# Performance work log

Hardware: AMD Instinct MI355X
Metric: run time of the kernel (lower is better)

Reference implementation:

```python
import jax, jax.numpy as jnp
import numpy as np

B, N, D, DN, F, NUM_F, O, H = 8, 4096, 256, 128, 128, 1024, 8, 1024
EPS = 1e-5

def setup_inputs() -> dict:
    key = jax.random.key(0)
    ks = jax.random.split(key, 10)
    s = 0.02
    x = jax.random.normal(ks[0], (B, N, D), dtype=jnp.float32)
    ctx = jax.random.normal(ks[1], (B, DN), dtype=jnp.float32)
    idx = jax.random.randint(ks[2], (F,), 0, NUM_F, dtype=jnp.int64)
    cond_w = jax.random.normal(ks[3], (DN, 2 * D), dtype=jnp.float32) * s
    cond_b = jnp.zeros((2 * D,), dtype=jnp.float32)
    ffn_w_in = jax.random.normal(ks[4], (D, 2 * H), dtype=jnp.float32) * s
    ffn_b_in = jnp.zeros((2 * H,), dtype=jnp.float32)
    ffn_w_out = jax.random.normal(ks[5], (H, D), dtype=jnp.float32) * s
    ffn_b_out = jnp.zeros((D,), dtype=jnp.float32)
    emb = jax.random.normal(ks[6], (NUM_F, D * O), dtype=jnp.float32) * s
    return {"x": x, "ctx": ctx, "idx": idx, "cond_w": cond_w, "cond_b": cond_b,
            "ffn_w_in": ffn_w_in, "ffn_b_in": ffn_b_in,
            "ffn_w_out": ffn_w_out, "ffn_b_out": ffn_b_out, "emb": emb}

def reference(x, ctx, idx, cond_w, cond_b, ffn_w_in, ffn_b_in, ffn_w_out, ffn_b_out, emb):
    # Conditional LayerNorm: normalize over last dim, FiLM-style modulation from ctx
    mu = jnp.mean(x, axis=-1, keepdims=True)
    var = jnp.mean((x - mu) ** 2, axis=-1, keepdims=True)
    h = (x - mu) * jax.lax.rsqrt(var + EPS)                      # [B,N,D]
    ss = ctx @ cond_w + cond_b                                   # [B,2D]
    scale, shift = jnp.split(ss, 2, axis=-1)                     # [B,D] each
    h = h * (1.0 + scale[:, None, :]) + shift[:, None, :]
    # Gated FFN: in-proj -> (gelu(gate) * value) -> out-proj
    uv = h @ ffn_w_in + ffn_b_in                                 # [B,N,2H]
    u, v = jnp.split(uv, 2, axis=-1)
    y = (jax.nn.gelu(u) * v) @ ffn_w_out + ffn_b_out             # [B,N,D]
    # Embedding-generated per-feature output weights, then batched contraction
    w = emb[idx].reshape(F, D, O)                                # gather [F,D,O]
    out = jnp.einsum('bnd,fdo->bnfo', y, w)                      # [B,N,F,O]
    return out
```

## Files before the change

### kernel.cpp

```cpp
#include <hip/hip_runtime.h>
#include <cstdint>
#include <cstddef>

#define M_TOT 32768
#define D_    256
#define DN_   128
#define TWO_D 512
#define H_    1024
#define TWO_H 2048

typedef unsigned short ushort_t;
typedef __attribute__((ext_vector_type(8))) short bf16x8;
typedef __attribute__((ext_vector_type(4))) float f32x4;

__device__ __forceinline__ ushort_t f2bf(float f) {
  union { float f; uint32_t i; } v; v.f = f;
  uint32_t r = v.i + 0x7fffu + ((v.i >> 16) & 1u);
  return (ushort_t)(r >> 16);
}

__device__ __forceinline__ void async_ld16(const void* g, void* l) {
  __builtin_amdgcn_global_load_lds(
      (const __attribute__((address_space(1))) void*)g,
      (__attribute__((address_space(3))) void*)l, 16, 0, 0);
}

__global__ __launch_bounds__(256) void cond_ss_kernel(
    const float* __restrict__ ctx, const float* __restrict__ cond_w,
    const float* __restrict__ cond_b, float* __restrict__ ss) {
  int j = blockIdx.x * 256 + threadIdx.x;
  int b = j >> 9, col = j & 511;
  float acc = cond_b[col];
  for (int k = 0; k < DN_; ++k)
    acc += ctx[b * DN_ + k] * cond_w[k * TWO_D + col];
  ss[j] = acc;
}

__global__ __launch_bounds__(256) void transpose_f32_bf16_kernel(
    const float* __restrict__ in, ushort_t* __restrict__ out, int R, int C) {
  __shared__ float T[64 * 65];
  int ctiles = C >> 6;
  int bi = blockIdx.x / ctiles, bj = blockIdx.x % ctiles;
  int r0 = bi * 64, c0 = bj * 64;
  int tid = threadIdx.x;
#pragma unroll
  for (int it = 0; it < 16; ++it) {
    int idx = it * 256 + tid;
    int r = idx >> 6, c = idx & 63;
    T[r * 65 + c] = in[(size_t)(r0 + r) * C + c0 + c];
  }
  __syncthreads();
#pragma unroll
  for (int it = 0; it < 8; ++it) {
    int idx = it * 256 + tid;
    int a = idx >> 5;
    int b = (idx & 31) * 2;
    uint32_t pk = (uint32_t)f2bf(T[b * 65 + a]) |
                  ((uint32_t)f2bf(T[(b + 1) * 65 + a]) << 16);
    *(uint32_t*)&out[(size_t)(c0 + a) * R + r0 + b] = pk;
  }
}

__global__ __launch_bounds__(256) void gather_emb_kernel(
    const float* __restrict__ emb, const int* __restrict__ idx,
    ushort_t* __restrict__ W2T) {
  int f = blockIdx.x;
  bool looks64 = (idx[1] == 0) & (idx[3] == 0) & (idx[5] == 0) & (idx[7] == 0);
  int fi = looks64 ? idx[2 * f] : idx[f];
  const float* src = emb + (size_t)fi * 2048;
  int o = threadIdx.x >> 5, d0 = (threadIdx.x & 31) * 8;
  ushort_t buf[8];
#pragma unroll
  for (int k = 0; k < 8; ++k) buf[k] = f2bf(src[(d0 + k) * 8 + o]);
  *(bf16x8*)&W2T[(size_t)(f * 8 + o) * 256 + d0] = *(bf16x8*)buf;
}

__global__ __launch_bounds__(256) void ln_film_kernel(
    const float* __restrict__ x, const float* __restrict__ ss,
    ushort_t* __restrict__ h) {
  int row = blockIdx.x * 4 + (threadIdx.x >> 6);
  int lane = threadIdx.x & 63;
  int b = row >> 12;
  const float* xr = x + (size_t)row * D_;
  float4 pk = *(const float4*)(xr + lane * 4);
  float f0 = pk.x, f1 = pk.y, f2 = pk.z, f3 = pk.w;
  float s = f0 + f1 + f2 + f3;
  float q = f0 * f0 + f1 * f1 + f2 * f2 + f3 * f3;
#pragma unroll
  for (int off = 32; off > 0; off >>= 1) {
    s += __shfl_xor(s, off, 64);
    q += __shfl_xor(q, off, 64);
  }
  float mean = s * (1.0f / 256.0f);
  float var = q * (1.0f / 256.0f) - mean * mean;
  float rs = rsqrtf(var + 1e-5f);
  int d = lane * 4;
  const float* ssb = ss + b * TWO_D;
  float o0 = (f0 - mean) * rs * (1.0f + ssb[d + 0]) + ssb[256 + d + 0];
  float o1 = (f1 - mean) * rs * (1.0f + ssb[d + 1]) + ssb[256 + d + 1];
  float o2 = (f2 - mean) * rs * (1.0f + ssb[d + 2]) + ssb[256 + d + 2];
  float o3 = (f3 - mean) * rs * (1.0f + ssb[d + 3]) + ssb[256 + d + 3];
  uint2 st;
  st.x = (uint32_t)f2bf(o0) | ((uint32_t)f2bf(o1) << 16);
  st.y = (uint32_t)f2bf(o2) | ((uint32_t)f2bf(o3) << 16);
  *(uint2*)(h + (size_t)row * D_ + lane * 4) = st;
}

__global__ __launch_bounds__(512, 2) void ffn_fused_kernel(
    const ushort_t* __restrict__ h,
    const ushort_t* __restrict__ WinT,
    const float* __restrict__ bin,
    const ushort_t* __restrict__ WoutT,
    const float* __restrict__ bout,
    ushort_t* __restrict__ y) {
  __shared__ ushort_t S3[3][8192];
  __shared__ ushort_t Gs[128 * 72];
  __shared__ float Lbin[2048];
  const int tid = threadIdx.x, lane = tid & 63, wave = tid >> 6;
  const int wm = wave >> 1, wn = wave & 1;
  const int r = lane >> 2, q = lane & 3;
  const int qs = q ^ ((r >> 1) & 3);
  const int l15 = lane & 15, l4 = lane >> 4;
  const int m0 = blockIdx.x * 128;
  const int fragoff = l15 * 32 + (l4 ^ ((l15 >> 1) & 3)) * 8;

  const char* winb  = (const char*)WinT  + r * 512 + qs * 16;
  const char* woutb = (const char*)WoutT + r * 2048 + qs * 16;

  const ushort_t* hp = h + (size_t)(m0 + wm * 32 + l15) * 256 + l4 * 8;
  bf16x8 a_reg[2][8];
#pragma unroll
  for (int rt = 0; rt < 2; ++rt)
#pragma unroll
    for (int kc = 0; kc < 8; ++kc)
      a_reg[rt][kc] = *(const bf16x8*)(hp + rt * 4096 + kc * 32);

  async_ld16((const char*)bin + wave * 1024 + lane * 16,
             (char*)Lbin + wave * 1024);

  auto stage_in = [&](ushort_t* dst, int jrow, int k0e) {
#pragma unroll
    for (int i = 0; i < 2; ++i) {
      int tt = i * 8 + wave;
      int vv = tt >> 3, t7 = tt & 7;
      int ks = t7 >> 2, cc = t7 & 3;
      async_ld16(winb + (size_t)vv * 524288 + jrow * 32768 + cc * 8192 +
                     k0e * 2 + ks * 64,
                 &dst[tt * 512]);
    }
  };
  auto stage_wout = [&](ushort_t* dst, int jrow, int s2) {
#pragma unroll
    for (int i = 0; i < 2; ++i) {
      int tt = i * 8 + wave;
      async_ld16(woutb + (size_t)tt * 32768 + jrow * 128 + s2 * 64,
                 &dst[tt * 512]);
    }
  };

  stage_in(S3[0], 0, 0);
  stage_in(S3[1], 0, 64);

  f32x4 yac[2][8] = {};

#define ENTRY2()                                        \
  asm volatile("s_waitcnt vmcnt(2)" ::: "memory");      \
  __builtin_amdgcn_s_barrier();                         \
  asm volatile("" ::: "memory");
#define ENTRY2L()                                                  \
  asm volatile("s_waitcnt vmcnt(2) lgkmcnt(0)" ::: "memory");      \
  __builtin_amdgcn_s_barrier();                                    \
  asm volatile("" ::: "memory");

#define MFMA_IN(buf, p_)                                                      \
  {                                                                           \
    const ushort_t* cur_ = (buf);                                             \
    __builtin_amdgcn_s_setprio(1);                                            \
    _Pragma("unroll")                                                         \
    for (int ks = 0; ks < 2; ++ks) {                                          \
      _Pragma("unroll")                                                       \
      for (int jj = 0; jj < 2; ++jj) {                                        \
        int tt = ks * 4 + wn * 2 + jj;                                        \
        bf16x8 bu = *(const bf16x8*)&cur_[tt * 512 + fragoff];                \
        bf16x8 bv = *(const bf16x8*)&cur_[(8 + tt) * 512 + fragoff];          \
        uac[0][jj] = __builtin_amdgcn_mfma_f32_16x16x32_bf16(a_reg[0][(p_)*2+ks], bu, uac[0][jj], 0, 0, 0); \
        uac[1][jj] = __builtin_amdgcn_mfma_f32_16x16x32_bf16(a_reg[1][(p_)*2+ks], bu, uac[1][jj], 0, 0, 0); \
        vac[0][jj] = __builtin_amdgcn_mfma_f32_16x16x32_bf16(a_reg[0][(p_)*2+ks], bv, vac[0][jj], 0, 0, 0); \
        vac[1][jj] = __builtin_amdgcn_mfma_f32_16x16x32_bf16(a_reg[1][(p_)*2+ks], bv, vac[1][jj], 0, 0, 0); \
      }                                                                       \
    }                                                                         \
    __builtin_amdgcn_s_setprio(0);                                            \
  }

#define MFMA_OUT(buf, s2_)                                                    \
  {                                                                           \
    const ushort_t* cur_ = (buf);                                             \
    bf16x8 gf0 = *(const bf16x8*)&Gs[(wm * 32 + l15) * 72 + (s2_) * 32 + l4 * 8];      \
    bf16x8 gf1 = *(const bf16x8*)&Gs[(wm * 32 + 16 + l15) * 72 + (s2_) * 32 + l4 * 8]; \
    __builtin_amdgcn_s_setprio(1);                                            \
    _Pragma("unroll")                                                         \
    for (int nt8 = 0; nt8 < 8; ++nt8) {                                       \
      bf16x8 bw = *(const bf16x8*)&cur_[(wn * 8 + nt8) * 512 + fragoff];      \
      yac[0][nt8] = __builtin_amdgcn_mfma_f32_16x16x32_bf16(gf0, bw, yac[0][nt8], 0, 0, 0); \
      yac[1][nt8] = __builtin_amdgcn_mfma_f32_16x16x32_bf16(gf1, bw, yac[1][nt8], 0, 0, 0); \
    }                                                                         \
    __builtin_amdgcn_s_setprio(0);                                            \
  }

  for (int j = 0; j < 16; ++j) {
    const int jn = (j + 1) & 15;
    f32x4 uac[2][2] = {}, vac[2][2] = {};

    ENTRY2(); stage_in(S3[2], j, 128);  MFMA_IN(S3[0], 0);
    ENTRY2(); stage_in(S3[0], j, 192);  MFMA_IN(S3[1], 1);
    ENTRY2(); stage_wout(S3[1], j, 0);  MFMA_IN(S3[2], 2);
    ENTRY2(); stage_wout(S3[2], j, 1);  MFMA_IN(S3[0], 3);

#pragma unroll
    for (int jj = 0; jj < 2; ++jj) {
      int gcol = wn * 32 + jj * 16 + l15;
      float bub = Lbin[j * 64 + gcol];
      float bvb = Lbin[1024 + j * 64 + gcol];
#pragma unroll
      for (int rt = 0; rt < 2; ++rt) {
#pragma unroll
        for (int rr = 0; rr < 4; ++rr) {
          float u = uac[rt][jj][rr] + bub;
          float v = vac[rt][jj][rr] + bvb;
          float t = 0.7978845608028654f * (u + 0.044715f * u * u * u);
          float e = __expf(2.0f * t);
          float th = 1.0f - 2.0f / (e + 1.0f);
          float gl = 0.5f * u * (1.0f + th);
          Gs[(wm * 32 + rt * 16 + l4 * 4 + rr) * 72 + gcol] = f2bf(gl * v);
        }
      }
    }

    ENTRY2L(); stage_in(S3[0], jn, 0);  MFMA_OUT(S3[1], 0);
    ENTRY2();  stage_in(S3[1], jn, 64); MFMA_OUT(S3[2], 1);
  }

  asm volatile("s_waitcnt vmcnt(0)" ::: "memory");
  __builtin_amdgcn_s_barrier();
  asm volatile("" ::: "memory");
  ushort_t* E = &S3[0][0];
#pragma unroll
  for (int hh = 0; hh < 2; ++hh) {
    if ((wm >> 1) == hh) {
      int er0 = (wm & 1) * 32;
#pragma unroll
      for (int nt8 = 0; nt8 < 8; ++nt8) {
        int col = wn * 128 + nt8 * 16 + l15;
        float bb = bout[col];
#pragma unroll
        for (int rt = 0; rt < 2; ++rt)
#pragma unroll
          for (int rr = 0; rr < 4; ++rr)
            E[(er0 + rt * 16 + l4 * 4 + rr) * 264 + col] = f2bf(yac[rt][nt8][rr] + bb);
      }
    }
    asm volatile("s_waitcnt lgkmcnt(0)" ::: "memory");
    __builtin_amdgcn_s_barrier();
    asm volatile("" ::: "memory");
#pragma unroll
    for (int it = 0; it < 4; ++it) {
      int id = it * 512 + tid;
      int rr = id >> 5, cc = id & 31;
      bf16x8 vv = *(const bf16x8*)&E[rr * 264 + cc * 8];
      *(bf16x8*)&y[(size_t)(m0 + hh * 64 + rr) * 256 + cc * 8] = vv;
    }
    if (hh == 0) {
      __builtin_amdgcn_s_barrier();
      asm volatile("" ::: "memory");
    }
  }
#undef ENTRY2
#undef ENTRY2L
#undef MFMA_IN
#undef MFMA_OUT
}

__global__ __launch_bounds__(256, 2) void gemm_out_kernel(
    const ushort_t* __restrict__ A, const ushort_t* __restrict__ BT,
    float* __restrict__ C) {
  __shared__ ushort_t SB[2][16384];
  const int tid = threadIdx.x, lane = tid & 63, wave = tid >> 6;
  const int wm = wave >> 1, wn = wave & 1;
  const int m0 = blockIdx.x * 128, n0 = blockIdx.y * 128;
  const int r = lane >> 2, q = lane & 3;
  const int qs = q ^ ((r >> 1) & 3);
  const int l15 = lane & 15, l4 = lane >> 4;
  const int fragoff = l15 * 32 + (l4 ^ ((l15 >> 1) & 3)) * 8;
  const int N = 1024, K = 256;

  auto stage = [&](ushort_t* dst, int k0) {
#pragma unroll
    for (int i = 0; i < 4; ++i) {
      int t = i * 4 + wave;
      int rt = t >> 1, ks = t & 1;
      async_ld16(A + (size_t)(m0 + rt * 16 + r) * K + k0 + ks * 32 + qs * 8, &dst[t * 512]);
      async_ld16(BT + (size_t)(n0 + rt * 16 + r) * K + k0 + ks * 32 + qs * 8, &dst[(16 + t) * 512]);
    }
  };

  f32x4 acc[4][4] = {};
  stage(SB[0], 0);
#pragma unroll
  for (int ki = 0; ki < 4; ++ki) {
    __builtin_amdgcn_s_barrier();
    asm volatile("" ::: "memory");
    if (ki < 3) {
      stage(SB[(ki + 1) & 1], (ki + 1) * 64);
      asm volatile("s_waitcnt vmcnt(8)" ::: "memory");
    } else {
      asm volatile("s_waitcnt vmcnt(0)" ::: "memory");
    }
    __builtin_amdgcn_s_barrier();
    asm volatile("" ::: "memory");
    const ushort_t* cur = SB[ki & 1];
    __builtin_amdgcn_s_setprio(1);
#pragma unroll
    for (int ks = 0; ks < 2; ++ks) {
      bf16x8 a[4], b[4];
#pragma unroll
      for (int i = 0; i < 4; ++i)
        a[i] = *(const bf16x8*)&cur[((wm * 4 + i) * 2 + ks) * 512 + fragoff];
#pragma unroll
      for (int jt = 0; jt < 4; ++jt)
        b[jt] = *(const bf16x8*)&cur[(16 + (wn * 4 + jt) * 2 + ks) * 512 + fragoff];
#pragma unroll
      for (int i = 0; i < 4; ++i)
#pragma unroll
        for (int jt = 0; jt < 4; ++jt)
          acc[i][jt] = __builtin_amdgcn_mfma_f32_16x16x32_bf16(a[i], b[jt], acc[i][jt], 0, 0, 0);
    }
    __builtin_amdgcn_s_setprio(0);
  }
#pragma unroll
  for (int jt = 0; jt < 4; ++jt) {
    int col = n0 + wn * 64 + jt * 16 + l15;
#pragma unroll
    for (int i = 0; i < 4; ++i) {
      int row = m0 + wm * 64 + i * 16 + l4 * 4;
#pragma unroll
      for (int rr = 0; rr < 4; ++rr)
        C[(size_t)(row + rr) * N + col] = acc[i][jt][rr];
    }
  }
}

extern "C" void kernel_launch(void* const* d_in, const int* in_sizes, int n_in,
                              void* d_out, int out_size, void* d_ws, size_t ws_size,
                              hipStream_t stream) {
  const float* x      = (const float*)d_in[0];
  const float* ctx    = (const float*)d_in[1];
  const int*   idx    = (const int*)d_in[2];
  const float* cond_w = (const float*)d_in[3];
  const float* cond_b = (const float*)d_in[4];
  const float* w_in   = (const float*)d_in[5];
  const float* b_in   = (const float*)d_in[6];
  const float* w_out  = (const float*)d_in[7];
  const float* b_out  = (const float*)d_in[8];
  const float* emb    = (const float*)d_in[9];

  char* w = (char*)d_ws;
  float* ss = (float*)w;           w += (size_t)8 * TWO_D * 4;
  ushort_t* h = (ushort_t*)w;      w += (size_t)M_TOT * D_ * 2;
  ushort_t* y = (ushort_t*)w;      w += (size_t)M_TOT * D_ * 2;
  ushort_t* WinT = (ushort_t*)w;   w += (size_t)TWO_H * D_ * 2;
  ushort_t* WoutT = (ushort_t*)w;  w += (size_t)D_ * H_ * 2;
  ushort_t* W2T = (ushort_t*)w;    w += (size_t)H_ * D_ * 2;

  cond_ss_kernel<<<16, 256, 0, stream>>>(ctx, cond_w, cond_b, ss);
  transpose_f32_bf16_kernel<<<(D_ / 64) * (TWO_H / 64), 256, 0, stream>>>(w_in, WinT, D_, TWO_H);
  transpose_f32_bf16_kernel<<<(H_ / 64) * (D_ / 64), 256, 0, stream>>>(w_out, WoutT, H_, D_);
  gather_emb_kernel<<<128, 256, 0, stream>>>(emb, idx, W2T);
  ln_film_kernel<<<M_TOT / 4, 256, 0, stream>>>(x, ss, h);
  ffn_fused_kernel<<<M_TOT / 128, 512, 0, stream>>>(h, WinT, b_in, WoutT, b_out, y);
  gemm_out_kernel<<<dim3(M_TOT / 128, H_ / 128), 256, 0, stream>>>(y, W2T, (float*)d_out);
}
```

Before: 292.9 us.

## Retile FFN waves to 2x4 grid and stage final GEMM output via LDS

Changes the FFN kernel's wave layout from 4x2 to 2x4, so each wave holds 64 rows of A in registers and covers fewer columns. This gives each B fragment load from LDS more MFMA reuse in both the in-projection and out-projection. It also rewrites the final contraction GEMM epilogue to stage fp32 accumulators through shared memory and write coalesced float4 rows, in place of scattered scalar stores. The cost is more A registers per wave (which may hurt occupancy at launch bounds 512,2) and extra barriers in the epilogue.

```diff
diff --git a/kernel.cpp b/kernel.cpp
--- a/kernel.cpp
+++ b/kernel.cpp
@@ -117,7 +117,7 @@
   __shared__ ushort_t Gs[128 * 72];
   __shared__ float Lbin[2048];
   const int tid = threadIdx.x, lane = tid & 63, wave = tid >> 6;
-  const int wm = wave >> 1, wn = wave & 1;
+  const int wm = wave >> 2, wn = wave & 3;
   const int r = lane >> 2, q = lane & 3;
   const int qs = q ^ ((r >> 1) & 3);
   const int l15 = lane & 15, l4 = lane >> 4;
@@ -127,10 +127,10 @@
   const char* winb  = (const char*)WinT  + r * 512 + qs * 16;
   const char* woutb = (const char*)WoutT + r * 2048 + qs * 16;
 
-  const ushort_t* hp = h + (size_t)(m0 + wm * 32 + l15) * 256 + l4 * 8;
-  bf16x8 a_reg[2][8];
-#pragma unroll
-  for (int rt = 0; rt < 2; ++rt)
+  const ushort_t* hp = h + (size_t)(m0 + wm * 64 + l15) * 256 + l4 * 8;
+  bf16x8 a_reg[4][8];
+#pragma unroll
+  for (int rt = 0; rt < 4; ++rt)
 #pragma unroll
     for (int kc = 0; kc < 8; ++kc)
       a_reg[rt][kc] = *(const bf16x8*)(hp + rt * 4096 + kc * 32);
@@ -161,7 +161,7 @@
   stage_in(S3[0], 0, 0);
   stage_in(S3[1], 0, 64);
 
-  f32x4 yac[2][8] = {};
+  f32x4 yac[4][4] = {};
 
 #define ENTRY2()                                        \
   asm volatile("s_waitcnt vmcnt(2)" ::: "memory");      \
@@ -178,15 +178,13 @@
     __builtin_amdgcn_s_setprio(1);                                            \
     _Pragma("unroll")                                                         \
     for (int ks = 0; ks < 2; ++ks) {                                          \
+      int tt = ks * 4 + wn;                                                   \
+      bf16x8 bu = *(const bf16x8*)&cur_[tt * 512 + fragoff];                  \
+      bf16x8 bv = *(const bf16x8*)&cur_[(8 + tt) * 512 + fragoff];            \
       _Pragma("unroll")                                                       \
-      for (int jj = 0; jj < 2; ++jj) {                                        \
-        int tt = ks * 4 + wn * 2 + jj;                                        \
-        bf16x8 bu = *(const bf16x8*)&cur_[tt * 512 + fragoff];                \
-        bf16x8 bv = *(const bf16x8*)&cur_[(8 + tt) * 512 + fragoff];          \
-        uac[0][jj] = __builtin_amdgcn_mfma_f32_16x16x32_bf16(a_reg[0][(p_)*2+ks], bu, uac[0][jj], 0, 0, 0); \
-        uac[1][jj] = __builtin_amdgcn_mfma_f32_16x16x32_bf16(a_reg[1][(p_)*2+ks], bu, uac[1][jj], 0, 0, 0); \
-        vac[0][jj] = __builtin_amdgcn_mfma_f32_16x16x32_bf16(a_reg[0][(p_)*2+ks], bv, vac[0][jj], 0, 0, 0); \
-        vac[1][jj] = __builtin_amdgcn_mfma_f32_16x16x32_bf16(a_reg[1][(p_)*2+ks], bv, vac[1][jj], 0, 0, 0); \
+      for (int rt = 0; rt < 4; ++rt) {                                        \
+        uac[rt] = __builtin_amdgcn_mfma_f32_16x16x32_bf16(a_reg[rt][(p_)*2+ks], bu, uac[rt], 0, 0, 0); \
+        vac[rt] = __builtin_amdgcn_mfma_f32_16x16x32_bf16(a_reg[rt][(p_)*2+ks], bv, vac[rt], 0, 0, 0); \
       }                                                                       \
     }                                                                         \
     __builtin_amdgcn_s_setprio(0);                                            \
@@ -195,43 +193,45 @@
 #define MFMA_OUT(buf, s2_)                                                    \
   {                                                                           \
     const ushort_t* cur_ = (buf);                                             \
-    bf16x8 gf0 = *(const bf16x8*)&Gs[(wm * 32 + l15) * 72 + (s2_) * 32 + l4 * 8];      \
-    bf16x8 gf1 = *(const bf16x8*)&Gs[(wm * 32 + 16 + l15) * 72 + (s2_) * 32 + l4 * 8]; \
+    bf16x8 gf[4];                                                             \
+    _Pragma("unroll")                                                         \
+    for (int rt = 0; rt < 4; ++rt)                                            \
+      gf[rt] = *(const bf16x8*)&Gs[(wm * 64 + rt * 16 + l15) * 72 + (s2_) * 32 + l4 * 8]; \
     __builtin_amdgcn_s_setprio(1);                                            \
     _Pragma("unroll")                                                         \
-    for (int nt8 = 0; nt8 < 8; ++nt8) {                                       \
-      bf16x8 bw = *(const bf16x8*)&cur_[(wn * 8 + nt8) * 512 + fragoff];      \
-      yac[0][nt8] = __builtin_amdgcn_mfma_f32_16x16x32_bf16(gf0, bw, yac[0][nt8], 0, 0, 0); \
-      yac[1][nt8] = __builtin_amdgcn_mfma_f32_16x16x32_bf16(gf1, bw, yac[1][nt8], 0, 0, 0); \
+    for (int nt = 0; nt < 4; ++nt) {                                          \
+      bf16x8 bw = *(const bf16x8*)&cur_[(wn * 4 + nt) * 512 + fragoff];       \
+      _Pragma("unroll")                                                       \
+      for (int rt = 0; rt < 4; ++rt)                                          \
+        yac[rt][nt] = __builtin_amdgcn_mfma_f32_16x16x32_bf16(gf[rt], bw, yac[rt][nt], 0, 0, 0); \
     }                                                                         \
     __builtin_amdgcn_s_setprio(0);                                            \
   }
 
   for (int j = 0; j < 16; ++j) {
     const int jn = (j + 1) & 15;
-    f32x4 uac[2][2] = {}, vac[2][2] = {};
+    f32x4 uac[4] = {}, vac[4] = {};
 
     ENTRY2(); stage_in(S3[2], j, 128);  MFMA_IN(S3[0], 0);
     ENTRY2(); stage_in(S3[0], j, 192);  MFMA_IN(S3[1], 1);
     ENTRY2(); stage_wout(S3[1], j, 0);  MFMA_IN(S3[2], 2);
     ENTRY2(); stage_wout(S3[2], j, 1);  MFMA_IN(S3[0], 3);
 
-#pragma unroll
-    for (int jj = 0; jj < 2; ++jj) {
-      int gcol = wn * 32 + jj * 16 + l15;
+    {
+      int gcol = wn * 16 + l15;
       float bub = Lbin[j * 64 + gcol];
       float bvb = Lbin[1024 + j * 64 + gcol];
 #pragma unroll
-      for (int rt = 0; rt < 2; ++rt) {
+      for (int rt = 0; rt < 4; ++rt) {
 #pragma unroll
         for (int rr = 0; rr < 4; ++rr) {
-          float u = uac[rt][jj][rr] + bub;
-          float v = vac[rt][jj][rr] + bvb;
+          float u = uac[rt][rr] + bub;
+          float v = vac[rt][rr] + bvb;
           float t = 0.7978845608028654f * (u + 0.044715f * u * u * u);
           float e = __expf(2.0f * t);
           float th = 1.0f - 2.0f / (e + 1.0f);
           float gl = 0.5f * u * (1.0f + th);
-          Gs[(wm * 32 + rt * 16 + l4 * 4 + rr) * 72 + gcol] = f2bf(gl * v);
+          Gs[(wm * 64 + rt * 16 + l4 * 4 + rr) * 72 + gcol] = f2bf(gl * v);
         }
       }
     }
@@ -246,17 +246,16 @@
   ushort_t* E = &S3[0][0];
 #pragma unroll
   for (int hh = 0; hh < 2; ++hh) {
-    if ((wm >> 1) == hh) {
-      int er0 = (wm & 1) * 32;
-#pragma unroll
-      for (int nt8 = 0; nt8 < 8; ++nt8) {
-        int col = wn * 128 + nt8 * 16 + l15;
+    if (wm == hh) {
+#pragma unroll
+      for (int nt = 0; nt < 4; ++nt) {
+        int col = wn * 64 + nt * 16 + l15;
         float bb = bout[col];
 #pragma unroll
-        for (int rt = 0; rt < 2; ++rt)
+        for (int rt = 0; rt < 4; ++rt)
 #pragma unroll
           for (int rr = 0; rr < 4; ++rr)
-            E[(er0 + rt * 16 + l4 * 4 + rr) * 264 + col] = f2bf(yac[rt][nt8][rr] + bb);
+            E[(rt * 16 + l4 * 4 + rr) * 264 + col] = f2bf(yac[rt][nt][rr] + bb);
       }
     }
     asm volatile("s_waitcnt lgkmcnt(0)" ::: "memory");
@@ -336,15 +335,33 @@
     }
     __builtin_amdgcn_s_setprio(0);
   }
-#pragma unroll
-  for (int jt = 0; jt < 4; ++jt) {
-    int col = n0 + wn * 64 + jt * 16 + l15;
-#pragma unroll
-    for (int i = 0; i < 4; ++i) {
-      int row = m0 + wm * 64 + i * 16 + l4 * 4;
-#pragma unroll
-      for (int rr = 0; rr < 4; ++rr)
-        C[(size_t)(row + rr) * N + col] = acc[i][jt][rr];
+  float* Cs = (float*)&SB[0][0];
+#pragma unroll
+  for (int p = 0; p < 2; ++p) {
+    __builtin_amdgcn_s_barrier();
+    asm volatile("" ::: "memory");
+    if (wm == p) {
+#pragma unroll
+      for (int jt = 0; jt < 4; ++jt) {
+        int col = wn * 64 + jt * 16 + l15;
+#pragma unroll
+        for (int i = 0; i < 4; ++i) {
+          int rl = i * 16 + (l4 << 2);
+#pragma unroll
+          for (int rr = 0; rr < 4; ++rr)
+            Cs[(rl + rr) * 132 + col] = acc[i][jt][rr];
+        }
+      }
+    }
+    asm volatile("s_waitcnt lgkmcnt(0)" ::: "memory");
+    __builtin_amdgcn_s_barrier();
+    asm volatile("" ::: "memory");
+#pragma unroll
+    for (int it = 0; it < 8; ++it) {
+      int t = it * 256 + tid;
+      int rr = t >> 5, c = (t & 31) * 4;
+      float4 v = *(const float4*)&Cs[rr * 132 + c];
+      *(float4*)&C[(size_t)(m0 + p * 64 + rr) * N + n0 + c] = v;
     }
   }
 }
```

After: 305.3 us. +4.2%, slower.

## Merge prep kernels and restructure output GEMM with coalesced LDS-staged stores

Applied to the files above, without the earlier changes.

The four small preprocessing kernels (cond projection, two weight transposes, embedding gather) become one launch, with blocks dispatched by index, to cut launch overhead. The output GEMM drops LDS double-buffered async staging and loads fragments straight from global memory. Each block now covers 64x256 instead of 128x128, and accumulators go through an LDS tile so the fp32 output is written as coalesced float4 rows rather than scattered scalar stores. The output write is the dominant traffic at 128 MB. The cost is more global read traffic for A/B fragments without LDS reuse, plus extra LDS round trips and barriers in the epilogue.

```diff
diff --git a/kernel.cpp b/kernel.cpp
--- a/kernel.cpp
+++ b/kernel.cpp
@@ -25,24 +25,12 @@
       (__attribute__((address_space(3))) void*)l, 16, 0, 0);
 }
 
-__global__ __launch_bounds__(256) void cond_ss_kernel(
-    const float* __restrict__ ctx, const float* __restrict__ cond_w,
-    const float* __restrict__ cond_b, float* __restrict__ ss) {
-  int j = blockIdx.x * 256 + threadIdx.x;
-  int b = j >> 9, col = j & 511;
-  float acc = cond_b[col];
-  for (int k = 0; k < DN_; ++k)
-    acc += ctx[b * DN_ + k] * cond_w[k * TWO_D + col];
-  ss[j] = acc;
-}
-
-__global__ __launch_bounds__(256) void transpose_f32_bf16_kernel(
-    const float* __restrict__ in, ushort_t* __restrict__ out, int R, int C) {
-  __shared__ float T[64 * 65];
+__device__ __forceinline__ void transpose_body(
+    const float* __restrict__ in, ushort_t* __restrict__ out, int R, int C,
+    int bb, int tid, float* T) {
   int ctiles = C >> 6;
-  int bi = blockIdx.x / ctiles, bj = blockIdx.x % ctiles;
+  int bi = bb / ctiles, bj = bb % ctiles;
   int r0 = bi * 64, c0 = bj * 64;
-  int tid = threadIdx.x;
 #pragma unroll
   for (int it = 0; it < 16; ++it) {
     int idx = it * 256 + tid;
@@ -61,18 +49,37 @@
   }
 }
 
-__global__ __launch_bounds__(256) void gather_emb_kernel(
+__global__ __launch_bounds__(256) void prep_kernel(
+    const float* __restrict__ ctx, const float* __restrict__ cond_w,
+    const float* __restrict__ cond_b, float* __restrict__ ss,
+    const float* __restrict__ w_in, ushort_t* __restrict__ WinT,
+    const float* __restrict__ w_out, ushort_t* __restrict__ WoutT,
     const float* __restrict__ emb, const int* __restrict__ idx,
     ushort_t* __restrict__ W2T) {
-  int f = blockIdx.x;
-  bool looks64 = (idx[1] == 0) & (idx[3] == 0) & (idx[5] == 0) & (idx[7] == 0);
-  int fi = looks64 ? idx[2 * f] : idx[f];
-  const float* src = emb + (size_t)fi * 2048;
-  int o = threadIdx.x >> 5, d0 = (threadIdx.x & 31) * 8;
-  ushort_t buf[8];
-#pragma unroll
-  for (int k = 0; k < 8; ++k) buf[k] = f2bf(src[(d0 + k) * 8 + o]);
-  *(bf16x8*)&W2T[(size_t)(f * 8 + o) * 256 + d0] = *(bf16x8*)buf;
+  __shared__ float T[64 * 65];
+  int bid = blockIdx.x, tid = threadIdx.x;
+  if (bid < 16) {
+    int j = bid * 256 + tid;
+    int b = j >> 9, col = j & 511;
+    float acc = cond_b[col];
+    for (int k = 0; k < DN_; ++k)
+      acc += ctx[b * DN_ + k] * cond_w[k * TWO_D + col];
+    ss[j] = acc;
+  } else if (bid < 144) {
+    transpose_body(w_in, WinT, D_, TWO_H, bid - 16, tid, T);
+  } else if (bid < 208) {
+    transpose_body(w_out, WoutT, H_, D_, bid - 144, tid, T);
+  } else {
+    int f = bid - 208;
+    bool looks64 = (idx[1] == 0) & (idx[3] == 0) & (idx[5] == 0) & (idx[7] == 0);
+    int fi = looks64 ? idx[2 * f] : idx[f];
+    const float* src = emb + (size_t)fi * 2048;
+    int o = tid >> 5, d0 = (tid & 31) * 8;
+    ushort_t buf[8];
+#pragma unroll
+    for (int k = 0; k < 8; ++k) buf[k] = f2bf(src[(d0 + k) * 8 + o]);
+    *(bf16x8*)&W2T[(size_t)(f * 8 + o) * 256 + d0] = *(bf16x8*)buf;
+  }
 }
 
 __global__ __launch_bounds__(256) void ln_film_kernel(
@@ -280,71 +287,54 @@
 #undef MFMA_OUT
 }
 
-__global__ __launch_bounds__(256, 2) void gemm_out_kernel(
+__global__ __launch_bounds__(256, 4) void gemm_out_kernel(
     const ushort_t* __restrict__ A, const ushort_t* __restrict__ BT,
     float* __restrict__ C) {
-  __shared__ ushort_t SB[2][16384];
+  __shared__ float Cs[32 * 260];
   const int tid = threadIdx.x, lane = tid & 63, wave = tid >> 6;
-  const int wm = wave >> 1, wn = wave & 1;
-  const int m0 = blockIdx.x * 128, n0 = blockIdx.y * 128;
-  const int r = lane >> 2, q = lane & 3;
-  const int qs = q ^ ((r >> 1) & 3);
   const int l15 = lane & 15, l4 = lane >> 4;
-  const int fragoff = l15 * 32 + (l4 ^ ((l15 >> 1) & 3)) * 8;
-  const int N = 1024, K = 256;
-
-  auto stage = [&](ushort_t* dst, int k0) {
-#pragma unroll
-    for (int i = 0; i < 4; ++i) {
-      int t = i * 4 + wave;
-      int rt = t >> 1, ks = t & 1;
-      async_ld16(A + (size_t)(m0 + rt * 16 + r) * K + k0 + ks * 32 + qs * 8, &dst[t * 512]);
-      async_ld16(BT + (size_t)(n0 + rt * 16 + r) * K + k0 + ks * 32 + qs * 8, &dst[(16 + t) * 512]);
-    }
-  };
-
+  const int m0 = blockIdx.y * 64;
+  const int n0 = blockIdx.x * 256;
+  const ushort_t* Ap = A + (size_t)(m0 + l15) * 256 + l4 * 8;
+  const ushort_t* Bp = BT + (size_t)(n0 + wave * 64 + l15) * 256 + l4 * 8;
   f32x4 acc[4][4] = {};
-  stage(SB[0], 0);
-#pragma unroll
-  for (int ki = 0; ki < 4; ++ki) {
-    __builtin_amdgcn_s_barrier();
-    asm volatile("" ::: "memory");
-    if (ki < 3) {
-      stage(SB[(ki + 1) & 1], (ki + 1) * 64);
-      asm volatile("s_waitcnt vmcnt(8)" ::: "memory");
-    } else {
-      asm volatile("s_waitcnt vmcnt(0)" ::: "memory");
-    }
-    __builtin_amdgcn_s_barrier();
-    asm volatile("" ::: "memory");
-    const ushort_t* cur = SB[ki & 1];
-    __builtin_amdgcn_s_setprio(1);
+#pragma unroll
+  for (int k0 = 0; k0 < 256; k0 += 64) {
 #pragma unroll
     for (int ks = 0; ks < 2; ++ks) {
       bf16x8 a[4], b[4];
 #pragma unroll
       for (int i = 0; i < 4; ++i)
-        a[i] = *(const bf16x8*)&cur[((wm * 4 + i) * 2 + ks) * 512 + fragoff];
+        a[i] = *(const bf16x8*)(Ap + i * 4096 + k0 + ks * 32);
 #pragma unroll
       for (int jt = 0; jt < 4; ++jt)
-        b[jt] = *(const bf16x8*)&cur[(16 + (wn * 4 + jt) * 2 + ks) * 512 + fragoff];
+        b[jt] = *(const bf16x8*)(Bp + jt * 4096 + k0 + ks * 32);
 #pragma unroll
       for (int i = 0; i < 4; ++i)
 #pragma unroll
         for (int jt = 0; jt < 4; ++jt)
           acc[i][jt] = __builtin_amdgcn_mfma_f32_16x16x32_bf16(a[i], b[jt], acc[i][jt], 0, 0, 0);
     }
-    __builtin_amdgcn_s_setprio(0);
-  }
-#pragma unroll
-  for (int jt = 0; jt < 4; ++jt) {
-    int col = n0 + wn * 64 + jt * 16 + l15;
-#pragma unroll
-    for (int i = 0; i < 4; ++i) {
-      int row = m0 + wm * 64 + i * 16 + l4 * 4;
-#pragma unroll
-      for (int rr = 0; rr < 4; ++rr)
-        C[(size_t)(row + rr) * N + col] = acc[i][jt][rr];
+  }
+#pragma unroll
+  for (int p = 0; p < 2; ++p) {
+    __syncthreads();
+#pragma unroll
+    for (int ii = 0; ii < 2; ++ii) {
+      int i = p * 2 + ii;
+#pragma unroll
+      for (int jt = 0; jt < 4; ++jt)
+#pragma unroll
+        for (int rr = 0; rr < 4; ++rr)
+          Cs[(ii * 16 + l4 * 4 + rr) * 260 + wave * 64 + jt * 16 + l15] = acc[i][jt][rr];
+    }
+    __syncthreads();
+#pragma unroll
+    for (int it = 0; it < 8; ++it) {
+      int id = it * 256 + tid;
+      int rr = id >> 6, c = (id & 63) * 4;
+      float4 v = *(const float4*)&Cs[rr * 260 + c];
+      *(float4*)&C[(size_t)(m0 + p * 32 + rr) * 1024 + n0 + c] = v;
     }
   }
 }
@@ -371,11 +361,9 @@
   ushort_t* WoutT = (ushort_t*)w;  w += (size_t)D_ * H_ * 2;
   ushort_t* W2T = (ushort_t*)w;    w += (size_t)H_ * D_ * 2;
 
-  cond_ss_kernel<<<16, 256, 0, stream>>>(ctx, cond_w, cond_b, ss);
-  transpose_f32_bf16_kernel<<<(D_ / 64) * (TWO_H / 64), 256, 0, stream>>>(w_in, WinT, D_, TWO_H);
-  transpose_f32_bf16_kernel<<<(H_ / 64) * (D_ / 64), 256, 0, stream>>>(w_out, WoutT, H_, D_);
-  gather_emb_kernel<<<128, 256, 0, stream>>>(emb, idx, W2T);
+  prep_kernel<<<336, 256, 0, stream>>>(ctx, cond_w, cond_b, ss,
+                                       w_in, WinT, w_out, WoutT, emb, idx, W2T);
   ln_film_kernel<<<M_TOT / 4, 256, 0, stream>>>(x, ss, h);
   ffn_fused_kernel<<<M_TOT / 128, 512, 0, stream>>>(h, WinT, b_in, WoutT, b_out, y);
-  gemm_out_kernel<<<dim3(M_TOT / 128, H_ / 128), 256, 0, stream>>>(y, W2T, (float*)d_out);
-}
+  gemm_out_kernel<<<dim3(4, 512), 256, 0, stream>>>(y, W2T, (float*)d_out);
+}
```

New measurement: 316.3 us. 8.0% more time.
